# Performance work log

Measured on AMD Instinct MI355X. Metric: run time of the kernel, lower is better.

## Reference

```python
import jax, jax.numpy as jnp
import numpy as np

B, L, D, M, H = 32, 4096, 512, 64, 8
HD = D // H  # head dim = 64
NEG = -1e9


def setup_inputs() -> dict:
    key = jax.random.key(0)
    ks = jax.random.split(key, 12)
    s = 1.0 / np.sqrt(D)
    return {
        "query_features": jax.random.normal(ks[0], (B, L, D), jnp.float32),
        "mask": jax.random.randint(ks[1], (B, L), 0, 2, jnp.int32),
        "memory": jax.random.normal(ks[2], (M, D), jnp.float32),
        "Wq": jax.random.normal(ks[3], (D, D), jnp.float32) * s,
        "bq": jax.random.normal(ks[4], (D,), jnp.float32) * 0.01,
        "Wk": jax.random.normal(ks[5], (D, D), jnp.float32) * s,
        "bk": jax.random.normal(ks[6], (D,), jnp.float32) * 0.01,
        "Wv": jax.random.normal(ks[7], (D, D), jnp.float32) * s,
        "bv": jax.random.normal(ks[8], (D,), jnp.float32) * 0.01,
        "Wo": jax.random.normal(ks[9], (D, D), jnp.float32) * s,
        "bo": jax.random.normal(ks[10], (D,), jnp.float32) * 0.01,
    }


def reference(query_features, mask, memory, Wq, bq, Wk, bk, Wv, bv, Wo, bo):
    # read_memory: MHA(query=features, key=value=memory broadcast over batch)
    # with additive attn_mask of -1e9 on rows whose query position is invalid
    # (torch masks every key for an invalid query -> uniform attention there).
    q = (query_features @ Wq.T + bq).reshape(B, L, H, HD)
    k = (memory @ Wk.T + bk).reshape(M, H, HD)   # shared across batch
    v = (memory @ Wv.T + bv).reshape(M, H, HD)
    scores = jnp.einsum('blhd,mhd->bhlm', q, k) / np.sqrt(HD)  # [B,H,L,M]
    bias = jnp.where(mask[:, None, :, None] == 0, NEG, 0.0).astype(scores.dtype)
    attn = jax.nn.softmax(scores + bias, axis=-1)
    ctx = jnp.einsum('bhlm,mhd->blhd', attn, v).reshape(B, L, D)
    return ctx @ Wo.T + bo
```

## Files before the change

kernel.cpp:

```cpp
#include <hip/hip_runtime.h>
#include <hip/hip_bf16.h>

#define DD 512
#define HDIM 64
#define NROWS 131072

typedef __bf16 bf16x8 __attribute__((ext_vector_type(8)));
typedef float f32x4 __attribute__((ext_vector_type(4)));
typedef __bf16 bf16x2 __attribute__((ext_vector_type(2)));

static __device__ __forceinline__ unsigned bfbits(float f) {
    union { float f; unsigned u; } x; x.f = f;
    unsigned r = x.u + 0x7fffu + ((x.u >> 16) & 1u);
    return r >> 16;
}
static __device__ __forceinline__ __bf16 to_bf16(float f) {
    union { unsigned short s; __bf16 b; } y; y.s = (unsigned short)bfbits(f); return y.b;
}
static __device__ __forceinline__ unsigned pk2(float lo, float hi) {
    bf16x2 t; t[0] = (__bf16)lo; t[1] = (__bf16)hi;
    union { bf16x2 b; unsigned u; } z; z.b = t; return z.u;
}

static __device__ __forceinline__ int imgoff(int p, int g, int e) {
    return p * 64 + ((((g) ^ ((p) & 3) ^ (((p) >> 2) & 3)) & 3) << 4) + e * 2;
}

static __device__ __forceinline__ size_t fragoff(int c, int d) {
    return (size_t)((((c >> 6) * 64 + (d >> 5) * 4 + ((c >> 4) & 3)) << 10)
         + (((((d >> 3) & 3) << 4) + (c & 15)) << 4) + ((d & 7) << 1));
}

static __device__ __forceinline__ void gll16(const void* gsrc, void* ldst) {
    __builtin_amdgcn_global_load_lds(
        (const __attribute__((address_space(1))) unsigned int*)gsrc,
        (__attribute__((address_space(3))) unsigned int*)ldst, 16, 0, 0);
}

#define VMCNT(n) asm volatile("s_waitcnt vmcnt(" #n ")" ::: "memory")
#define LGKM0 asm volatile("s_waitcnt lgkmcnt(0)" ::: "memory")
#define MEMPIN asm volatile("" ::: "memory")

static __device__ __forceinline__ int xcd_swz(int bid, int nwg) {
    const int q = nwg >> 3, r = nwg & 7;
    const int xcd = bid & 7, idx = bid >> 3;
    return (xcd < r ? xcd * (q + 1) : r * (q + 1) + (xcd - r) * q) + idx;
}

__global__ __launch_bounds__(256) void prep_kv(
    const float* __restrict__ memory,
    const float* __restrict__ Wk, const float* __restrict__ bk,
    const float* __restrict__ Wv, const float* __restrict__ bv,
    float* __restrict__ kproj, float* __restrict__ vproj) {
    __shared__ float memLds[64 * 65];
    __shared__ float wLds[32 * 65];
    const int t = threadIdx.x;
    const int b = blockIdx.x;
    const int mat = b >> 4;
    const int j0 = (b & 15) * 32;
    const float* W = mat ? Wv : Wk;
    const float* bias = mat ? bv : bk;
    float* proj = mat ? vproj : kproj;

    const int jloc = t >> 3;
    const int mbase = t & 7;
    float acc[8] = {0.f, 0.f, 0.f, 0.f, 0.f, 0.f, 0.f, 0.f};

    for (int dt = 0; dt < 8; ++dt) {
        const int d0 = dt * 64;
        __syncthreads();
        #pragma unroll
        for (int r = 0; r < 16; ++r) {
            const int row = r * 4 + (t >> 6);
            const int dd = t & 63;
            memLds[row * 65 + dd] = memory[(size_t)row * DD + d0 + dd];
        }
        #pragma unroll
        for (int r = 0; r < 8; ++r) {
            const int row = r * 4 + (t >> 6);
            const int dd = t & 63;
            wLds[row * 65 + dd] = W[(size_t)(j0 + row) * DD + d0 + dd];
        }
        __syncthreads();
        for (int d = 0; d < 64; ++d) {
            const float wv = wLds[jloc * 65 + d];
            #pragma unroll
            for (int i = 0; i < 8; ++i)
                acc[i] += memLds[(mbase + i * 8) * 65 + d] * wv;
        }
    }
    const float bj = bias[j0 + jloc];
    #pragma unroll
    for (int i = 0; i < 8; ++i)
        proj[(size_t)(mbase + i * 8) * DD + j0 + jloc] = acc[i] + bj;
}

__global__ __launch_bounds__(256) void prep_w(
    const float* __restrict__ Wq, const float* __restrict__ bq,
    const float* __restrict__ Wo,
    const float* __restrict__ kproj, const float* __restrict__ vproj,
    char* __restrict__ W2img, float* __restrict__ b2,
    char* __restrict__ W3fr) {
    __shared__ float aLds[64 * 65];
    __shared__ float bLds[64 * 65];
    const int t = threadIdx.x;
    const int b = blockIdx.x;

    if (b < 32) {
        const int h = b >> 2, dq = b & 3;
        #pragma unroll
        for (int r = 0; r < 16; ++r) {
            const int row = r * 4 + (t >> 6), col = t & 63;
            aLds[row * 65 + col] = kproj[(size_t)row * DD + h * 64 + col];
        }
        __syncthreads();
        if (dq == 0 && t < 64) {
            float s = 0.f;
            for (int hd = 0; hd < 64; ++hd) s += bq[h * 64 + hd] * aLds[t * 65 + hd];
            b2[h * 64 + t] = s;
        }
        for (int dt = 0; dt < 2; ++dt) {
            const int d0 = dq * 128 + dt * 64;
            __syncthreads();
            #pragma unroll
            for (int r = 0; r < 16; ++r) {
                const int row = r * 4 + (t >> 6), col = t & 63;
                bLds[row * 65 + col] = Wq[(size_t)(h * 64 + row) * DD + d0 + col];
            }
            __syncthreads();
            #pragma unroll
            for (int uu = 0; uu < 2; ++uu) {
                const int u = t + 256 * uu;
                const int m = u & 63, oct = u >> 6;
                float acc[8] = {0.f, 0.f, 0.f, 0.f, 0.f, 0.f, 0.f, 0.f};
                for (int hd = 0; hd < 64; ++hd) {
                    const float kv = aLds[m * 65 + hd];
                    #pragma unroll
                    for (int e = 0; e < 8; ++e)
                        acc[e] += kv * bLds[hd * 65 + oct * 8 + e];
                }
                const int d = d0 + oct * 8;
                bf16x8 v;
                #pragma unroll
                for (int e = 0; e < 8; ++e) v[e] = to_bf16(acc[e]);
                *(bf16x8*)(W2img + (size_t)(d >> 5) * 32768
                           + imgoff(h * 64 + m, (d >> 3) & 3, 0)) = v;
            }
        }
    } else {
        const int hc = (b - 32) >> 2, jq = (b - 32) & 3;
        #pragma unroll
        for (int r = 0; r < 16; ++r) {
            const int row = r * 4 + (t >> 6), col = t & 63;
            aLds[row * 65 + col] = vproj[(size_t)row * DD + hc * 64 + col];
        }
        for (int jt = 0; jt < 2; ++jt) {
            const int j0 = jq * 128 + jt * 64;
            __syncthreads();
            #pragma unroll
            for (int r = 0; r < 16; ++r) {
                const int row = r * 4 + (t >> 6), col = t & 63;
                bLds[row * 65 + col] = Wo[(size_t)(j0 + row) * DD + hc * 64 + col];
            }
            __syncthreads();
            #pragma unroll
            for (int uu = 0; uu < 2; ++uu) {
                const int u = t + 256 * uu;
                const int jl = u & 63, w = u >> 6;
                const int blk = w >> 2, oct = w & 3;
                float acc[8] = {0.f, 0.f, 0.f, 0.f, 0.f, 0.f, 0.f, 0.f};
                for (int hd = 0; hd < 64; ++hd) {
                    const float wv = bLds[jl * 65 + hd];
                    #pragma unroll
                    for (int e = 0; e < 8; ++e) {
                        const int s = oct * 8 + e;
                        const int cl = (s >> 1) + ((s & 1) << 4);
                        acc[e] += wv * aLds[(blk * 32 + cl) * 65 + hd];
                    }
                }
                const int cp0 = hc * 64 + blk * 32 + oct * 8;
                bf16x8 v;
                #pragma unroll
                for (int e = 0; e < 8; ++e) v[e] = to_bf16(acc[e]);
                *(bf16x8*)(W3fr + fragoff(j0 + jl, cp0)) = v;
            }
        }
    }
}

__global__ __launch_bounds__(256, 2) void attn_fused(
    const float* __restrict__ x, const int* __restrict__ mask,
    const char* __restrict__ W2img, const float* __restrict__ b2,
    const char* __restrict__ W3fr, const float* __restrict__ bo,
    float* __restrict__ out) {
    __shared__ char ldsb[73728];

    const int tid = threadIdx.x;
    const int lane = tid & 63;
    const int wn = tid >> 6;
    const int lc = lane & 15, grp = lane >> 4;
    const int swz = xcd_swz(blockIdx.x, gridDim.x);
    const int gr0 = swz * 64;

    const int arow = tid >> 2, ag = tid & 3;
    const float* asrc = x + (size_t)(gr0 + arow) * DD + ag * 8;
    const int adst = imgoff(arow, ag, 0);
    const char* bsrc = W2img + wn * 8192 + lane * 16;

    f32x4 sreg[2][2];
    #define ALOAD(kt, set)                                                         \
        { sreg[set][0] = __builtin_nontemporal_load((const f32x4*)(asrc + (kt) * 32));     \
          sreg[set][1] = __builtin_nontemporal_load((const f32x4*)(asrc + (kt) * 32 + 4)); }
    #define AWRITE(buf, set)                                                       \
        { uint4 u;                                                                 \
          u.x = pk2(sreg[set][0][0], sreg[set][0][1]);                             \
          u.y = pk2(sreg[set][0][2], sreg[set][0][3]);                             \
          u.z = pk2(sreg[set][1][0], sreg[set][1][1]);                             \
          u.w = pk2(sreg[set][1][2], sreg[set][1][3]);                             \
          *(uint4*)(ldsb + (buf) * 4096 + adst) = u; }
    #define BGLL(kt, buf)                                                          \
        { _Pragma("unroll")                                                        \
          for (int g = 0; g < 8; ++g)                                              \
              gll16(bsrc + (size_t)(kt) * 32768 + g * 1024,                        \
                    ldsb + 8192 + (buf) * 32768 + wn * 8192 + g * 1024); }
    #define LDA1(buf, m)                                                           \
        (*(const bf16x8*)(ldsb + (buf) * 4096 + ((m) * 16 + lc) * 64               \
            + (((grp ^ (lc & 3) ^ (((m) * 4 + (lc >> 2)) & 3)) & 3) << 4)))
    #define LDB1(buf, n)                                                           \
        (*(const bf16x8*)(ldsb + 8192 + (buf) * 32768                              \
            + (wn * 128 + (n) * 16 + lc) * 64                                      \
            + (((grp ^ (lc & 3) ^ (((n) * 4 + (lc >> 2)) & 3)) & 3) << 4)))

    f32x4 acc[4][8];
    #pragma unroll
    for (int m = 0; m < 4; ++m)
        #pragma unroll
        for (int n = 0; n < 8; ++n) acc[m][n] = (f32x4){0.f, 0.f, 0.f, 0.f};

    BGLL(0, 0);
    MEMPIN;
    ALOAD(0, 0);
    MEMPIN;
    ALOAD(1, 1);
    VMCNT(2);
    AWRITE(0, 0);
    LGKM0;
    __builtin_amdgcn_s_barrier();
    __builtin_amdgcn_sched_barrier(0);

    #pragma unroll
    for (int s = 0; s < 16; ++s) {
        const int p = s & 1;
        if (s < 15) BGLL(s + 1, p ^ 1);
        MEMPIN;
        if (s < 14) ALOAD(s + 2, s & 1);
        bf16x8 af[4], bf[8];
        #pragma unroll
        for (int m = 0; m < 4; ++m) af[m] = LDA1(p, m);
        #pragma unroll
        for (int n = 0; n < 8; ++n) bf[n] = LDB1(p, n);
        __builtin_amdgcn_s_setprio(1);
        #pragma unroll
        for (int m = 0; m < 4; ++m)
            #pragma unroll
            for (int n = 0; n < 8; ++n)
                acc[m][n] = __builtin_amdgcn_mfma_f32_16x16x32_bf16(af[m], bf[n], acc[m][n], 0, 0, 0);
        __builtin_amdgcn_s_setprio(0);
        if (s < 14) {
            VMCNT(2);
            AWRITE(p ^ 1, (s + 1) & 1);
            LGKM0;
            __builtin_amdgcn_s_barrier();
            __builtin_amdgcn_sched_barrier(0);
        } else if (s < 15) {
            VMCNT(0);
            AWRITE(p ^ 1, 1);
            LGKM0;
            __builtin_amdgcn_s_barrier();
            __builtin_amdgcn_sched_barrier(0);
        }
    }
    __syncthreads();
    #undef ALOAD
    #undef AWRITE
    #undef BGLL
    #undef LDA1
    #undef LDB1

    const char* b3 = W3fr + wn * 131072 + lane * 16;
    #define LB3(kt, buf)                                                           \
        { _Pragma("unroll")                                                        \
          for (int n = 0; n < 8; ++n)                                              \
              bb3[buf][n] = *(const bf16x8*)(b3 + ((n) >> 2) * 65536               \
                  + (size_t)(kt) * 4096 + ((n) & 3) * 1024); }
    bf16x8 bb3[2][8];
    LB3(0, 0);

    float b2v[8];
    #pragma unroll
    for (int n = 0; n < 8; ++n) b2v[n] = b2[wn * 128 + n * 16 + lc];

    #pragma unroll
    for (int m = 0; m < 4; ++m) {
        const int4 mv = *(const int4*)(mask + gr0 + m * 16 + grp * 4);
        const int mk[4] = {mv.x, mv.y, mv.z, mv.w};
        #pragma unroll
        for (int hl = 0; hl < 2; ++hl) {
            #pragma unroll
            for (int j = 0; j < 4; ++j) {
                float s0 = (acc[m][hl * 4 + 0][j] + b2v[hl * 4 + 0]) * 0.125f;
                float s1 = (acc[m][hl * 4 + 1][j] + b2v[hl * 4 + 1]) * 0.125f;
                float s2 = (acc[m][hl * 4 + 2][j] + b2v[hl * 4 + 2]) * 0.125f;
                float s3 = (acc[m][hl * 4 + 3][j] + b2v[hl * 4 + 3]) * 0.125f;
                float mx = fmaxf(fmaxf(s0, s1), fmaxf(s2, s3));
                mx = fmaxf(mx, __shfl_xor(mx, 1));
                mx = fmaxf(mx, __shfl_xor(mx, 2));
                mx = fmaxf(mx, __shfl_xor(mx, 4));
                mx = fmaxf(mx, __shfl_xor(mx, 8));
                float p0 = __expf(s0 - mx);
                float p1 = __expf(s1 - mx);
                float p2 = __expf(s2 - mx);
                float p3 = __expf(s3 - mx);
                float sm = (p0 + p1) + (p2 + p3);
                sm += __shfl_xor(sm, 1);
                sm += __shfl_xor(sm, 2);
                sm += __shfl_xor(sm, 4);
                sm += __shfl_xor(sm, 8);
                float a0, a1, a2, a3;
                if (mk[j] == 0) {
                    a0 = a1 = a2 = a3 = 0.015625f;
                } else {
                    const float inv = 1.0f / sm;
                    a0 = p0 * inv; a1 = p1 * inv; a2 = p2 * inv; a3 = p3 * inv;
                }
                const int rl = m * 16 + grp * 4 + j;
                const int gp = ((lc >> 2) ^ (rl & 3) ^ ((rl >> 2) & 3)) & 3;
                const int base = 8192 + rl * 64 + (gp << 4) + (lc & 3) * 4;
                const int si0 = wn * 4 + hl * 2;
                *(unsigned*)(ldsb + base + si0 * 4096)       = pk2(a0, a1);
                *(unsigned*)(ldsb + base + (si0 + 1) * 4096) = pk2(a2, a3);
            }
        }
    }
    __syncthreads();

    #define LDA3(s, m)                                                             \
        (*(const bf16x8*)(ldsb + 8192 + (s) * 4096 + ((m) * 16 + lc) * 64          \
            + (((grp ^ (lc & 3) ^ (((m) * 4 + (lc >> 2)) & 3)) & 3) << 4)))

    #pragma unroll
    for (int m = 0; m < 4; ++m)
        #pragma unroll
        for (int n = 0; n < 8; ++n) acc[m][n] = (f32x4){0.f, 0.f, 0.f, 0.f};

    #pragma unroll
    for (int s = 0; s < 16; ++s) {
        const int p = s & 1;
        if (s < 15) LB3(s + 1, p ^ 1);
        bf16x8 af[4];
        #pragma unroll
        for (int m = 0; m < 4; ++m) af[m] = LDA3(s, m);
        __builtin_amdgcn_s_setprio(1);
        #pragma unroll
        for (int m = 0; m < 4; ++m)
            #pragma unroll
            for (int n = 0; n < 8; ++n)
                acc[m][n] = __builtin_amdgcn_mfma_f32_16x16x32_bf16(af[m], bb3[p][n], acc[m][n], 0, 0, 0);
        __builtin_amdgcn_s_setprio(0);
    }
    #undef LB3
    #undef LDA3

    float bov[8];
    #pragma unroll
    for (int n = 0; n < 8; ++n) bov[n] = bo[wn * 128 + n * 16 + lc];

    #pragma unroll
    for (int m = 0; m < 4; ++m) {
        #pragma unroll
        for (int j = 0; j < 4; ++j) {
            const int gr = gr0 + m * 16 + grp * 4 + j;
            float* orow = out + (size_t)gr * DD + wn * 128 + lc;
            #pragma unroll
            for (int n = 0; n < 8; ++n)
                __builtin_nontemporal_store(acc[m][n][j] + bov[n], orow + n * 16);
        }
    }
}

extern "C" void kernel_launch(void* const* d_in, const int* in_sizes, int n_in,
                              void* d_out, int out_size, void* d_ws, size_t ws_size,
                              hipStream_t stream) {
    const float* qf     = (const float*)d_in[0];
    const int*   mask   = (const int*)d_in[1];
    const float* memory = (const float*)d_in[2];
    const float* Wq     = (const float*)d_in[3];
    const float* bq     = (const float*)d_in[4];
    const float* Wk     = (const float*)d_in[5];
    const float* bk     = (const float*)d_in[6];
    const float* Wv     = (const float*)d_in[7];
    const float* bv     = (const float*)d_in[8];
    const float* Wo     = (const float*)d_in[9];
    const float* bo     = (const float*)d_in[10];

    char* ws = (char*)d_ws;
    float* kproj = (float*)ws;
    float* vproj = (float*)(ws + 131072);
    float* b2    = (float*)(ws + 262144);
    char*  W2img = ws + 264192;
    char*  W3fr  = ws + 788480;

    prep_kv<<<32, 256, 0, stream>>>(memory, Wk, bk, Wv, bv, kproj, vproj);
    prep_w<<<64, 256, 0, stream>>>(Wq, bq, Wo, kproj, vproj, W2img, b2, W3fr);
    attn_fused<<<NROWS / 64, 256, 0, stream>>>(qf, mask, W2img, b2, W3fr, bo, (float*)d_out);
}
```

Measured before the change: 278.4 us.

## Stage full X tile in LDS upfront and load W2 fragments directly to registers

The first GEMM (X times the folded Wq·K weights) no longer streams B tiles through LDS with global_load_lds and a per-step barrier pipeline. Instead, the whole 64x512 X tile is converted to bf16 and written to LDS once. The W2 weights are now pre-laid out in MFMA fragment order so each wave can load its B operands straight into registers with double buffering, matching the scheme the third GEMM already uses. This removes the per-k-step barriers and shrinks LDS from 72KB to 64KB, which may help occupancy. The cost is that the X load is no longer overlapped with compute, and global-to-register B loads rely on cache reuse across blocks.

```diff
diff --git a/kernel.cpp b/kernel.cpp
--- a/kernel.cpp
+++ b/kernel.cpp
@@ -30,16 +30,6 @@
     return (size_t)((((c >> 6) * 64 + (d >> 5) * 4 + ((c >> 4) & 3)) << 10)
          + (((((d >> 3) & 3) << 4) + (c & 15)) << 4) + ((d & 7) << 1));
 }
-
-static __device__ __forceinline__ void gll16(const void* gsrc, void* ldst) {
-    __builtin_amdgcn_global_load_lds(
-        (const __attribute__((address_space(1))) unsigned int*)gsrc,
-        (__attribute__((address_space(3))) unsigned int*)ldst, 16, 0, 0);
-}
-
-#define VMCNT(n) asm volatile("s_waitcnt vmcnt(" #n ")" ::: "memory")
-#define LGKM0 asm volatile("s_waitcnt lgkmcnt(0)" ::: "memory")
-#define MEMPIN asm volatile("" ::: "memory")
 
 static __device__ __forceinline__ int xcd_swz(int bid, int nwg) {
     const int q = nwg >> 3, r = nwg & 7;
@@ -99,7 +89,7 @@
     const float* __restrict__ Wq, const float* __restrict__ bq,
     const float* __restrict__ Wo,
     const float* __restrict__ kproj, const float* __restrict__ vproj,
-    char* __restrict__ W2img, float* __restrict__ b2,
+    char* __restrict__ W2fr, float* __restrict__ b2,
     char* __restrict__ W3fr) {
     __shared__ float aLds[64 * 65];
     __shared__ float bLds[64 * 65];
@@ -143,8 +133,7 @@
                 bf16x8 v;
                 #pragma unroll
                 for (int e = 0; e < 8; ++e) v[e] = to_bf16(acc[e]);
-                *(bf16x8*)(W2img + (size_t)(d >> 5) * 32768
-                           + imgoff(h * 64 + m, (d >> 3) & 3, 0)) = v;
+                *(bf16x8*)(W2fr + fragoff(h * 64 + m, d)) = v;
             }
         }
     } else {
@@ -190,10 +179,10 @@
 
 __global__ __launch_bounds__(256, 2) void attn_fused(
     const float* __restrict__ x, const int* __restrict__ mask,
-    const char* __restrict__ W2img, const float* __restrict__ b2,
+    const char* __restrict__ W2fr, const float* __restrict__ b2,
     const char* __restrict__ W3fr, const float* __restrict__ bo,
     float* __restrict__ out) {
-    __shared__ char ldsb[73728];
+    __shared__ char ldsb[65536];
 
     const int tid = threadIdx.x;
     const int lane = tid & 63;
@@ -202,97 +191,65 @@
     const int swz = xcd_swz(blockIdx.x, gridDim.x);
     const int gr0 = swz * 64;
 
-    const int arow = tid >> 2, ag = tid & 3;
-    const float* asrc = x + (size_t)(gr0 + arow) * DD + ag * 8;
-    const int adst = imgoff(arow, ag, 0);
-    const char* bsrc = W2img + wn * 8192 + lane * 16;
-
-    f32x4 sreg[2][2];
-    #define ALOAD(kt, set)                                                         \
-        { sreg[set][0] = __builtin_nontemporal_load((const f32x4*)(asrc + (kt) * 32));     \
-          sreg[set][1] = __builtin_nontemporal_load((const f32x4*)(asrc + (kt) * 32 + 4)); }
-    #define AWRITE(buf, set)                                                       \
-        { uint4 u;                                                                 \
-          u.x = pk2(sreg[set][0][0], sreg[set][0][1]);                             \
-          u.y = pk2(sreg[set][0][2], sreg[set][0][3]);                             \
-          u.z = pk2(sreg[set][1][0], sreg[set][1][1]);                             \
-          u.w = pk2(sreg[set][1][2], sreg[set][1][3]);                             \
-          *(uint4*)(ldsb + (buf) * 4096 + adst) = u; }
-    #define BGLL(kt, buf)                                                          \
+    {
+        const int gg = tid & 63;
+        const int si = gg >> 2, g = gg & 3;
+        #pragma unroll
+        for (int it = 0; it < 16; ++it) {
+            const int r = it * 4 + (tid >> 6);
+            const float* px = x + (size_t)(gr0 + r) * DD + gg * 8;
+            const f32x4 lo = __builtin_nontemporal_load((const f32x4*)px);
+            const f32x4 hi = __builtin_nontemporal_load((const f32x4*)(px + 4));
+            uint4 u;
+            u.x = pk2(lo[0], lo[1]); u.y = pk2(lo[2], lo[3]);
+            u.z = pk2(hi[0], hi[1]); u.w = pk2(hi[2], hi[3]);
+            *(uint4*)(ldsb + si * 4096 + imgoff(r, g, 0)) = u;
+        }
+    }
+    __syncthreads();
+
+    const char* b1 = W2fr + wn * 131072 + lane * 16;
+    const char* b3 = W3fr + wn * 131072 + lane * 16;
+    #define LB1(kt, buf)                                                           \
         { _Pragma("unroll")                                                        \
-          for (int g = 0; g < 8; ++g)                                              \
-              gll16(bsrc + (size_t)(kt) * 32768 + g * 1024,                        \
-                    ldsb + 8192 + (buf) * 32768 + wn * 8192 + g * 1024); }
-    #define LDA1(buf, m)                                                           \
-        (*(const bf16x8*)(ldsb + (buf) * 4096 + ((m) * 16 + lc) * 64               \
-            + (((grp ^ (lc & 3) ^ (((m) * 4 + (lc >> 2)) & 3)) & 3) << 4)))
-    #define LDB1(buf, n)                                                           \
-        (*(const bf16x8*)(ldsb + 8192 + (buf) * 32768                              \
-            + (wn * 128 + (n) * 16 + lc) * 64                                      \
-            + (((grp ^ (lc & 3) ^ (((n) * 4 + (lc >> 2)) & 3)) & 3) << 4)))
-
-    f32x4 acc[4][8];
-    #pragma unroll
-    for (int m = 0; m < 4; ++m)
-        #pragma unroll
-        for (int n = 0; n < 8; ++n) acc[m][n] = (f32x4){0.f, 0.f, 0.f, 0.f};
-
-    BGLL(0, 0);
-    MEMPIN;
-    ALOAD(0, 0);
-    MEMPIN;
-    ALOAD(1, 1);
-    VMCNT(2);
-    AWRITE(0, 0);
-    LGKM0;
-    __builtin_amdgcn_s_barrier();
-    __builtin_amdgcn_sched_barrier(0);
-
-    #pragma unroll
-    for (int s = 0; s < 16; ++s) {
-        const int p = s & 1;
-        if (s < 15) BGLL(s + 1, p ^ 1);
-        MEMPIN;
-        if (s < 14) ALOAD(s + 2, s & 1);
-        bf16x8 af[4], bf[8];
-        #pragma unroll
-        for (int m = 0; m < 4; ++m) af[m] = LDA1(p, m);
-        #pragma unroll
-        for (int n = 0; n < 8; ++n) bf[n] = LDB1(p, n);
-        __builtin_amdgcn_s_setprio(1);
-        #pragma unroll
-        for (int m = 0; m < 4; ++m)
-            #pragma unroll
-            for (int n = 0; n < 8; ++n)
-                acc[m][n] = __builtin_amdgcn_mfma_f32_16x16x32_bf16(af[m], bf[n], acc[m][n], 0, 0, 0);
-        __builtin_amdgcn_s_setprio(0);
-        if (s < 14) {
-            VMCNT(2);
-            AWRITE(p ^ 1, (s + 1) & 1);
-            LGKM0;
-            __builtin_amdgcn_s_barrier();
-            __builtin_amdgcn_sched_barrier(0);
-        } else if (s < 15) {
-            VMCNT(0);
-            AWRITE(p ^ 1, 1);
-            LGKM0;
-            __builtin_amdgcn_s_barrier();
-            __builtin_amdgcn_sched_barrier(0);
-        }
-    }
-    __syncthreads();
-    #undef ALOAD
-    #undef AWRITE
-    #undef BGLL
-    #undef LDA1
-    #undef LDB1
-
-    const char* b3 = W3fr + wn * 131072 + lane * 16;
+          for (int n = 0; n < 8; ++n)                                              \
+              bb1[buf][n] = *(const bf16x8*)(b1 + ((n) >> 2) * 65536               \
+                  + (size_t)(kt) * 4096 + ((n) & 3) * 1024); }
     #define LB3(kt, buf)                                                           \
         { _Pragma("unroll")                                                        \
           for (int n = 0; n < 8; ++n)                                              \
               bb3[buf][n] = *(const bf16x8*)(b3 + ((n) >> 2) * 65536               \
                   + (size_t)(kt) * 4096 + ((n) & 3) * 1024); }
+    #define LDIMG(s, m)                                                            \
+        (*(const bf16x8*)(ldsb + (s) * 4096 + ((m) * 16 + lc) * 64                 \
+            + (((grp ^ (lc & 3) ^ (((m) * 4 + (lc >> 2)) & 3)) & 3) << 4)))
+
+    f32x4 acc[4][8];
+    #pragma unroll
+    for (int m = 0; m < 4; ++m)
+        #pragma unroll
+        for (int n = 0; n < 8; ++n) acc[m][n] = (f32x4){0.f, 0.f, 0.f, 0.f};
+
+    bf16x8 bb1[2][8];
+    LB1(0, 0);
+    #pragma unroll
+    for (int s = 0; s < 16; ++s) {
+        const int p = s & 1;
+        if (s < 15) LB1(s + 1, p ^ 1);
+        bf16x8 af[4];
+        #pragma unroll
+        for (int m = 0; m < 4; ++m) af[m] = LDIMG(s, m);
+        __builtin_amdgcn_s_setprio(1);
+        #pragma unroll
+        for (int m = 0; m < 4; ++m)
+            #pragma unroll
+            for (int n = 0; n < 8; ++n)
+                acc[m][n] = __builtin_amdgcn_mfma_f32_16x16x32_bf16(af[m], bb1[p][n], acc[m][n], 0, 0, 0);
+        __builtin_amdgcn_s_setprio(0);
+    }
+    #undef LB1
+    __syncthreads();
+
     bf16x8 bb3[2][8];
     LB3(0, 0);
 
@@ -335,7 +292,7 @@
                 }
                 const int rl = m * 16 + grp * 4 + j;
                 const int gp = ((lc >> 2) ^ (rl & 3) ^ ((rl >> 2) & 3)) & 3;
-                const int base = 8192 + rl * 64 + (gp << 4) + (lc & 3) * 4;
+                const int base = rl * 64 + (gp << 4) + (lc & 3) * 4;
                 const int si0 = wn * 4 + hl * 2;
                 *(unsigned*)(ldsb + base + si0 * 4096)       = pk2(a0, a1);
                 *(unsigned*)(ldsb + base + (si0 + 1) * 4096) = pk2(a2, a3);
@@ -343,10 +300,6 @@
         }
     }
     __syncthreads();
-
-    #define LDA3(s, m)                                                             \
-        (*(const bf16x8*)(ldsb + 8192 + (s) * 4096 + ((m) * 16 + lc) * 64          \
-            + (((grp ^ (lc & 3) ^ (((m) * 4 + (lc >> 2)) & 3)) & 3) << 4)))
 
     #pragma unroll
     for (int m = 0; m < 4; ++m)
@@ -359,7 +312,7 @@
         if (s < 15) LB3(s + 1, p ^ 1);
         bf16x8 af[4];
         #pragma unroll
-        for (int m = 0; m < 4; ++m) af[m] = LDA3(s, m);
+        for (int m = 0; m < 4; ++m) af[m] = LDIMG(s, m);
         __builtin_amdgcn_s_setprio(1);
         #pragma unroll
         for (int m = 0; m < 4; ++m)
@@ -369,7 +322,7 @@
         __builtin_amdgcn_s_setprio(0);
     }
     #undef LB3
-    #undef LDA3
+    #undef LDIMG
 
     float bov[8];
     #pragma unroll
@@ -407,10 +360,10 @@
     float* kproj = (float*)ws;
     float* vproj = (float*)(ws + 131072);
     float* b2    = (float*)(ws + 262144);
-    char*  W2img = ws + 264192;
+    char*  W2fr  = ws + 264192;
     char*  W3fr  = ws + 788480;
 
     prep_kv<<<32, 256, 0, stream>>>(memory, Wk, bk, Wv, bv, kproj, vproj);
-    prep_w<<<64, 256, 0, stream>>>(Wq, bq, Wo, kproj, vproj, W2img, b2, W3fr);
-    attn_fused<<<NROWS / 64, 256, 0, stream>>>(qf, mask, W2img, b2, W3fr, bo, (float*)d_out);
-}
+    prep_w<<<64, 256, 0, stream>>>(Wq, bq, Wo, kproj, vproj, W2fr, b2, W3fr);
+    attn_fused<<<NROWS / 64, 256, 0, stream>>>(qf, mask, W2fr, b2, W3fr, bo, (float*)d_out);
+}
```

After: 261.5 us. -6.1%, faster.
